# Performance work log

Measured on AMD Instinct MI355X. Metric: run time of the kernel, lower is better.

## Reference

```python
import jax, jax.numpy as jnp
import numpy as np

B, T, N, H = 512, 128, 128, 256


def setup_inputs() -> dict:
    key = jax.random.key(0)
    ks = jax.random.split(key, 8)
    rn = lambda k, shape, sc: (jax.random.normal(k, shape, jnp.float32) * sc)
    return {
        "data": rn(ks[0], (B, T, N), 1.0),
        "h0": jnp.zeros((B, H), jnp.float32),
        # SimpleRNNCell params: h_t = tanh(x@Wx + h@Wh + b)
        "Wx": rn(ks[1], (N, H), 0.05),
        "Wh": rn(ks[2], (H, H), 0.05),
        "b": jnp.zeros((H,), jnp.float32),
        # InputAttention: w1: Dense(T) over last dim T; w2: Dense(T) over hidden; v: Dense(1)
        "W1": rn(ks[3], (T, T), 0.05),
        "b1": jnp.zeros((T,), jnp.float32),
        "W2": rn(ks[4], (H, T), 0.05),
        "b2": jnp.zeros((T,), jnp.float32),
        "Wv": rn(ks[5], (T, 1), 0.05),
        "bv": jnp.zeros((1,), jnp.float32),
        "n": N,
    }


def reference(data, h0, Wx, Wh, b, W1, b1, W2, b2, Wv, bv, n):
    # data: (B, T, n); h0: (B, H)
    Tlen = data.shape[1]
    x_perm = jnp.swapaxes(data, 1, 2)          # (B, n, T) == Permute((2,1))(x)
    pre = x_perm @ W1 + b1                      # w1(x_perm): loop-invariant, hoisted

    def step(h, x_t):
        # SimpleRNNCell: new state used for this step's attention
        h_new = jnp.tanh(x_t @ Wx + h @ Wh + b)                 # (B, H)
        q = h_new @ W2 + b2                                      # w2(RepeatVector(n)(h)) per row -> (B, T)
        score = jnp.tanh(pre + q[:, None, :])                    # (B, n, T)
        e = score @ Wv + bv                                      # (B, n, 1)
        e = jnp.swapaxes(e, 1, 2)                                # Permute((2,1)) -> (B, 1, n)
        alpha = jax.nn.softmax(e, axis=-1)                       # softmax over n
        return h_new, alpha

    xs = jnp.swapaxes(data, 0, 1)               # (T, B, n): data[:, t, :] per step
    _, alphas = jax.lax.scan(step, h0, xs)      # (T, B, 1, n)
    # faithful to tf.reshape(alpha_seq.stack(), (-1, T, n))
    alpha_seq = alphas.reshape(-1, Tlen, n)     # (B, T, n)
    return data * alpha_seq
```

## Files before the change

### kernel.cpp

```cpp
#include <hip/hip_runtime.h>


#define C2L 2.8853900817779268f
#define L2E 1.4426950408889634f

typedef _Float16 hf;
typedef _Float16 hf2 __attribute__((ext_vector_type(2)));
typedef _Float16 hf4 __attribute__((ext_vector_type(4)));
typedef _Float16 hf8 __attribute__((ext_vector_type(8)));
typedef float f32x4 __attribute__((ext_vector_type(4)));

__device__ __forceinline__ float fast_exp2(float x){
#if __has_builtin(__builtin_amdgcn_exp2f)
  return __builtin_amdgcn_exp2f(x);
#else
  return exp2f(x);
#endif
}
__device__ __forceinline__ float fast_rcp(float x){
#if __has_builtin(__builtin_amdgcn_rcpf)
  return __builtin_amdgcn_rcpf(x);
#else
  return 1.f/x;
#endif
}
__device__ __forceinline__ float dot2f(hf2 a, hf2 b, float c){
#if __has_builtin(__builtin_amdgcn_fdot2)
  return __builtin_amdgcn_fdot2(a, b, c, false);
#else
  return c + (float)a.x*(float)b.x + (float)a.y*(float)b.y;
#endif
}

__global__ __launch_bounds__(256) void k_prep_w(const float* __restrict__ Wx,
    const float* __restrict__ W2, const float* __restrict__ W1,
    hf* __restrict__ wts){
  int tid = blockIdx.x*256 + threadIdx.x;
  if (tid < 32768){
    int n = tid >> 7, k = tid & 127;
    wts[tid] = (hf)Wx[k*256 + n];
  } else if (tid < 65536){
    int t2 = tid - 32768;
    int n = t2 >> 8, k = t2 & 255;
    wts[tid] = (hf)W2[k*128 + n];
  } else {
    int t3 = tid - 65536;
    int n = t3 >> 7, k = t3 & 127;
    wts[tid] = (hf)W1[k*128 + n];
  }
}

template<int K, int MODE>
__global__ __launch_bounds__(256) void k_gemm(const void* __restrict__ Asrc,
    const hf* __restrict__ Bt, const float* __restrict__ bias,
    float* __restrict__ Cout){
  constexpr int SA = 136;
  __shared__ alignas(16) hf As[64*SA];
  __shared__ alignas(16) hf Bs[128*SA];
  const int tid = threadIdx.x;
  const int w = tid >> 6, lane = tid & 63;
  const int c = lane & 15, q = lane >> 4;
  const int bx = blockIdx.x;
  const int col0 = (MODE==0) ? blockIdx.y*128 : 0;

  float br[8];
  #pragma unroll
  for (int ni=0; ni<8; ni++) br[ni] = bias[col0 + ni*16 + c];

  f32x4 acc[8];
  #pragma unroll
  for (int ni=0; ni<8; ni++) acc[ni] = (f32x4){0.f,0.f,0.f,0.f};

  for (int kc=0; kc<K/128; kc++){
    if (MODE == 0){
      const float* A = (const float*)Asrc + (long)bx*64*128;
      #pragma unroll
      for (int v=0; v<8; v++){
        int f4 = v*256 + tid;
        int m = f4 >> 5, k4 = (f4 & 31)*4;
        float4 d = *(const float4*)&A[m*128 + k4];
        hf4 h = {(hf)d.x,(hf)d.y,(hf)d.z,(hf)d.w};
        *(hf4*)&As[m*SA + k4] = h;
      }
    } else if (MODE == 1){
      const hf* A = (const hf*)Asrc + (long)bx*64*256;
      #pragma unroll
      for (int v=0; v<4; v++){
        int f8 = v*256 + tid;
        int m = f8 >> 4, k8 = (f8 & 15)*8;
        *(hf8*)&As[m*SA + k8] = *(const hf8*)&A[m*256 + kc*128 + k8];
      }
    } else {
      const float* A = (const float*)Asrc + (long)(bx>>1)*16384;
      const int i0 = (bx & 1)*64;
      #pragma unroll
      for (int v=0; v<8; v++){
        int f4 = v*256 + tid;
        int t = f4 >> 4, i4 = (f4 & 15)*4;
        float4 d = *(const float4*)&A[t*128 + i0 + i4];
        As[(i4+0)*SA + t] = (hf)d.x;
        As[(i4+1)*SA + t] = (hf)d.y;
        As[(i4+2)*SA + t] = (hf)d.z;
        As[(i4+3)*SA + t] = (hf)d.w;
      }
    }
    #pragma unroll
    for (int v=0; v<8; v++){
      int f8 = v*256 + tid;
      int n = f8 >> 4, k8 = (f8 & 15)*8;
      *(hf8*)&Bs[n*SA + k8] = *(const hf8*)&Bt[(col0+n)*K + kc*128 + k8];
    }
    __syncthreads();
    #pragma unroll
    for (int kk=0; kk<4; kk++){
      hf8 a = *(const hf8*)&As[(w*16 + c)*SA + kk*32 + q*8];
      #pragma unroll
      for (int ni=0; ni<8; ni++){
        hf8 b = *(const hf8*)&Bs[(ni*16 + c)*SA + kk*32 + q*8];
        acc[ni] = __builtin_amdgcn_mfma_f32_16x16x32_f16(a, b, acc[ni], 0, 0, 0);
      }
    }
    __syncthreads();
  }
  #pragma unroll
  for (int ni=0; ni<8; ni++){
    #pragma unroll
    for (int r=0; r<4; r++){
      int rloc = w*16 + q*4 + r;
      int col = col0 + ni*16 + c;
      float val = acc[ni][r] + br[ni];
      int addr;
      if (MODE == 0){
        int R = bx*64 + rloc;
        int b_ = R >> 7, t_ = R & 127;
        addr = (t_*512 + b_)*256 + col;
      } else if (MODE == 1){
        int R = bx*64 + rloc;
        addr = R*128 + col;
        val = fast_exp2(C2L*val);
      } else {
        int b_ = bx >> 1, i_ = (bx & 1)*64 + rloc;
        addr = b_*16384 + i_*128 + col;
        val = fast_exp2(C2L*val);
      }
      Cout[addr] = val;
    }
  }
}

__global__ __launch_bounds__(512) void k_rnn(const float* __restrict__ h0,
    const float* __restrict__ Wh, const float* __restrict__ xw,
    hf* __restrict__ Hb){
  __shared__ alignas(16) hf h_s[2][2][256];
  const int tid = threadIdx.x;
  const int j = tid & 255, beta = tid >> 8;
  const int bb = blockIdx.x*2 + beta;
  hf2 wreg[128];
  #pragma unroll
  for (int m=0;m<128;m++){
    float w0 = Wh[(2*m)*256 + j];
    float w1 = Wh[(2*m+1)*256 + j];
    wreg[m] = (hf2){(hf)w0, (hf)w1};
  }
  h_s[0][beta][j] = (hf)h0[bb*256 + j];
  float z = xw[(0*512 + bb)*256 + j];
  __syncthreads();
  for (int t=0;t<128;t++){
    int p = t & 1;
    float zn = (t < 127) ? xw[((t+1)*512 + bb)*256 + j] : 0.f;
    const hf2* hp = (const hf2*)(&h_s[p][beta][0]);
    float a0=0.f,a1=0.f,a2=0.f,a3=0.f;
    #pragma unroll
    for (int m=0;m<128;m+=4){
      a0 = dot2f(wreg[m],   hp[m],   a0);
      a1 = dot2f(wreg[m+1], hp[m+1], a1);
      a2 = dot2f(wreg[m+2], hp[m+2], a2);
      a3 = dot2f(wreg[m+3], hp[m+3], a3);
    }
    float v = z + ((a0+a1)+(a2+a3));
    float e2 = fast_exp2(v*C2L);
    float hn = 1.f - 2.f*fast_rcp(e2 + 1.f);
    Hb[(t*512+bb)*256 + j] = (hf)hn;
    h_s[p^1][beta][j] = (hf)hn;
    z = zn;
    __syncthreads();
  }
}

__global__ __launch_bounds__(256, 4) void k_attn(const float* __restrict__ P,
    const float* __restrict__ Qm, const float* __restrict__ Wv,
    const float* __restrict__ data, float* __restrict__ out){
  __shared__ alignas(16) float qs[32*128];
  __shared__ alignas(16) float wvs[128];
  __shared__ alignas(16) float epart[2][2][2][128];
  __shared__ float red[2][2][2];
  const int b = blockIdx.x, tile = blockIdx.y;
  const int tid = threadIdx.x;
  const int i = tid & 127, hl = tid >> 7;
  const int t0 = tile*32;
  if (tid < 128) wvs[tid] = -2.f*Wv[tid];
  #pragma unroll
  for (int v=0; v<4; v++){
    int flat = v*1024 + tid*4;
    int tt = flat >> 7, c = flat & 127;
    *(float4*)&qs[flat] = *(const float4*)&Qm[((t0+tt)*512 + b)*128 + c];
  }
  float4 p4[16];
  const float* prow = P + b*16384 + i*128 + hl*64;
  #pragma unroll
  for (int v=0; v<16; v++) p4[v] = *(const float4*)&prow[v*4];
  __syncthreads();
  for (int tp=0; tp<16; tp++){
    const int pp = tp & 1;
    const float* q0r = &qs[(2*tp)*128   + hl*64];
    const float* q1r = &qs[(2*tp+1)*128 + hl*64];
    const float* wvr = &wvs[hl*64];
    float4 acc0 = {0.f,0.f,0.f,0.f}, acc1 = {0.f,0.f,0.f,0.f};
    #pragma unroll
    for (int m=0; m<16; m++){
      float4 Pv = p4[m];
      float4 q0 = *(const float4*)&q0r[m*4];
      float4 q1 = *(const float4*)&q1r[m*4];
      float4 wv = *(const float4*)&wvr[m*4];
      float r0x = fast_rcp(fmaf(Pv.x, q0.x, 1.f));
      float r0y = fast_rcp(fmaf(Pv.y, q0.y, 1.f));
      float r0z = fast_rcp(fmaf(Pv.z, q0.z, 1.f));
      float r0w = fast_rcp(fmaf(Pv.w, q0.w, 1.f));
      float r1x = fast_rcp(fmaf(Pv.x, q1.x, 1.f));
      float r1y = fast_rcp(fmaf(Pv.y, q1.y, 1.f));
      float r1z = fast_rcp(fmaf(Pv.z, q1.z, 1.f));
      float r1w = fast_rcp(fmaf(Pv.w, q1.w, 1.f));
      acc0.x = fmaf(wv.x, r0x, acc0.x);
      acc0.y = fmaf(wv.y, r0y, acc0.y);
      acc0.z = fmaf(wv.z, r0z, acc0.z);
      acc0.w = fmaf(wv.w, r0w, acc0.w);
      acc1.x = fmaf(wv.x, r1x, acc1.x);
      acc1.y = fmaf(wv.y, r1y, acc1.y);
      acc1.z = fmaf(wv.z, r1z, acc1.z);
      acc1.w = fmaf(wv.w, r1w, acc1.w);
    }
    epart[pp][0][hl][i] = (acc0.x+acc0.y)+(acc0.z+acc0.w);
    epart[pp][1][hl][i] = (acc1.x+acc1.y)+(acc1.z+acc1.w);
    __syncthreads();
    const int tpar = tid >> 7;
    float e = epart[pp][tpar][0][i] + epart[pp][tpar][1][i];
    float pexp = fast_exp2(e*L2E);
    float sm = pexp;
    #pragma unroll
    for (int off=32; off; off>>=1) sm += __shfl_xor(sm, off);
    if ((tid & 63) == 0) red[pp][tpar][(tid>>6)&1] = sm;
    __syncthreads();
    float ssum = red[pp][tpar][0] + red[pp][tpar][1];
    float alpha = pexp * fast_rcp(ssum);
    int t = t0 + 2*tp + tpar;
    int base = (t*512 + b)*128 + i;
    out[base] = data[base]*alpha;
  }
}

extern "C" void kernel_launch(void* const* d_in, const int* in_sizes, int n_in,
                              void* d_out, int out_size, void* d_ws, size_t ws_size,
                              hipStream_t stream) {
  const float* data = (const float*)d_in[0];
  const float* h0   = (const float*)d_in[1];
  const float* Wx   = (const float*)d_in[2];
  const float* Wh   = (const float*)d_in[3];
  const float* bb   = (const float*)d_in[4];
  const float* W1   = (const float*)d_in[5];
  const float* b1   = (const float*)d_in[6];
  const float* W2   = (const float*)d_in[7];
  const float* b2   = (const float*)d_in[8];
  const float* Wv   = (const float*)d_in[9];
  float* wsp = (float*)d_ws;
  float* P   = wsp;
  float* xwQ = wsp + 8388608;
  hf*    Hbf = (hf*)(wsp + 25165824);
  hf*    wts = (hf*)(wsp + 33554432);
  const hf* Wxt = wts;
  const hf* W2t = wts + 32768;
  const hf* W1t = wts + 65536;
  float* out = (float*)d_out;

  hipLaunchKernelGGL(k_prep_w, dim3(320), dim3(256), 0, stream, Wx, W2, W1, wts);
  hipLaunchKernelGGL((k_gemm<128,0>), dim3(1024,2), dim3(256), 0, stream,
                     (const void*)data, Wxt, bb, xwQ);
  hipLaunchKernelGGL((k_gemm<128,2>), dim3(1024),   dim3(256), 0, stream,
                     (const void*)data, W1t, b1, P);
  hipLaunchKernelGGL(k_rnn, dim3(256), dim3(512), 0, stream, h0, Wh, xwQ, Hbf);
  hipLaunchKernelGGL((k_gemm<256,1>), dim3(1024),   dim3(256), 0, stream,
                     (const void*)Hbf, W2t, b2, xwQ);
  hipLaunchKernelGGL(k_attn, dim3(512, 4), dim3(256), 0, stream, P, xwQ, Wv, data, out);
}
```

Baseline: 399.2 us.

## Split RNN to one batch per block and pair reciprocals in attention

Result: faster. 385.5 us (-3.4%).

```diff
diff --git a/kernel.cpp b/kernel.cpp
--- a/kernel.cpp
+++ b/kernel.cpp
@@ -148,13 +148,12 @@
   }
 }
 
-__global__ __launch_bounds__(512) void k_rnn(const float* __restrict__ h0,
+__global__ __launch_bounds__(256, 3) void k_rnn(const float* __restrict__ h0,
     const float* __restrict__ Wh, const float* __restrict__ xw,
     hf* __restrict__ Hb){
-  __shared__ alignas(16) hf h_s[2][2][256];
-  const int tid = threadIdx.x;
-  const int j = tid & 255, beta = tid >> 8;
-  const int bb = blockIdx.x*2 + beta;
+  __shared__ alignas(16) hf h_s[2][256];
+  const int j = threadIdx.x;
+  const int bb = blockIdx.x;
   hf2 wreg[128];
   #pragma unroll
   for (int m=0;m<128;m++){
@@ -162,26 +161,31 @@
     float w1 = Wh[(2*m+1)*256 + j];
     wreg[m] = (hf2){(hf)w0, (hf)w1};
   }
-  h_s[0][beta][j] = (hf)h0[bb*256 + j];
+  h_s[0][j] = (hf)h0[bb*256 + j];
   float z = xw[(0*512 + bb)*256 + j];
   __syncthreads();
   for (int t=0;t<128;t++){
     int p = t & 1;
     float zn = (t < 127) ? xw[((t+1)*512 + bb)*256 + j] : 0.f;
-    const hf2* hp = (const hf2*)(&h_s[p][beta][0]);
-    float a0=0.f,a1=0.f,a2=0.f,a3=0.f;
-    #pragma unroll
-    for (int m=0;m<128;m+=4){
-      a0 = dot2f(wreg[m],   hp[m],   a0);
-      a1 = dot2f(wreg[m+1], hp[m+1], a1);
-      a2 = dot2f(wreg[m+2], hp[m+2], a2);
-      a3 = dot2f(wreg[m+3], hp[m+3], a3);
-    }
-    float v = z + ((a0+a1)+(a2+a3));
+    const hf8* h8 = (const hf8*)(&h_s[p][0]);
+    float a[8];
+    #pragma unroll
+    for (int u=0;u<8;u++) a[u]=0.f;
+    #pragma unroll
+    for (int mm=0; mm<32; mm++){
+      hf8 hv = h8[mm];
+      hf2 h0p = {hv[0],hv[1]}, h1p = {hv[2],hv[3]};
+      hf2 h2p = {hv[4],hv[5]}, h3p = {hv[6],hv[7]};
+      a[(4*mm+0)&7] = dot2f(wreg[4*mm+0], h0p, a[(4*mm+0)&7]);
+      a[(4*mm+1)&7] = dot2f(wreg[4*mm+1], h1p, a[(4*mm+1)&7]);
+      a[(4*mm+2)&7] = dot2f(wreg[4*mm+2], h2p, a[(4*mm+2)&7]);
+      a[(4*mm+3)&7] = dot2f(wreg[4*mm+3], h3p, a[(4*mm+3)&7]);
+    }
+    float v = z + (((a[0]+a[1])+(a[2]+a[3])) + ((a[4]+a[5])+(a[6]+a[7])));
     float e2 = fast_exp2(v*C2L);
     float hn = 1.f - 2.f*fast_rcp(e2 + 1.f);
     Hb[(t*512+bb)*256 + j] = (hf)hn;
-    h_s[p^1][beta][j] = (hf)hn;
+    h_s[p^1][j] = (hf)hn;
     z = zn;
     __syncthreads();
   }
@@ -192,8 +196,8 @@
     const float* __restrict__ data, float* __restrict__ out){
   __shared__ alignas(16) float qs[32*128];
   __shared__ alignas(16) float wvs[128];
-  __shared__ alignas(16) float epart[2][2][2][128];
-  __shared__ float red[2][2][2];
+  __shared__ alignas(16) float epart[2][2][4][128];
+  __shared__ float red[2][4][2];
   const int b = blockIdx.x, tile = blockIdx.y;
   const int tid = threadIdx.x;
   const int i = tid & 127, hl = tid >> 7;
@@ -210,51 +214,82 @@
   #pragma unroll
   for (int v=0; v<16; v++) p4[v] = *(const float4*)&prow[v*4];
   __syncthreads();
-  for (int tp=0; tp<16; tp++){
+  for (int tp=0; tp<8; tp++){
     const int pp = tp & 1;
-    const float* q0r = &qs[(2*tp)*128   + hl*64];
-    const float* q1r = &qs[(2*tp+1)*128 + hl*64];
+    const float* q0r = &qs[(4*tp)*128   + hl*64];
+    const float* q1r = &qs[(4*tp+1)*128 + hl*64];
+    const float* q2r = &qs[(4*tp+2)*128 + hl*64];
+    const float* q3r = &qs[(4*tp+3)*128 + hl*64];
     const float* wvr = &wvs[hl*64];
-    float4 acc0 = {0.f,0.f,0.f,0.f}, acc1 = {0.f,0.f,0.f,0.f};
+    float acc0=0.f, acc1=0.f, acc2=0.f, acc3=0.f;
     #pragma unroll
     for (int m=0; m<16; m++){
       float4 Pv = p4[m];
-      float4 q0 = *(const float4*)&q0r[m*4];
-      float4 q1 = *(const float4*)&q1r[m*4];
       float4 wv = *(const float4*)&wvr[m*4];
-      float r0x = fast_rcp(fmaf(Pv.x, q0.x, 1.f));
-      float r0y = fast_rcp(fmaf(Pv.y, q0.y, 1.f));
-      float r0z = fast_rcp(fmaf(Pv.z, q0.z, 1.f));
-      float r0w = fast_rcp(fmaf(Pv.w, q0.w, 1.f));
-      float r1x = fast_rcp(fmaf(Pv.x, q1.x, 1.f));
-      float r1y = fast_rcp(fmaf(Pv.y, q1.y, 1.f));
-      float r1z = fast_rcp(fmaf(Pv.z, q1.z, 1.f));
-      float r1w = fast_rcp(fmaf(Pv.w, q1.w, 1.f));
-      acc0.x = fmaf(wv.x, r0x, acc0.x);
-      acc0.y = fmaf(wv.y, r0y, acc0.y);
-      acc0.z = fmaf(wv.z, r0z, acc0.z);
-      acc0.w = fmaf(wv.w, r0w, acc0.w);
-      acc1.x = fmaf(wv.x, r1x, acc1.x);
-      acc1.y = fmaf(wv.y, r1y, acc1.y);
-      acc1.z = fmaf(wv.z, r1z, acc1.z);
-      acc1.w = fmaf(wv.w, r1w, acc1.w);
-    }
-    epart[pp][0][hl][i] = (acc0.x+acc0.y)+(acc0.z+acc0.w);
-    epart[pp][1][hl][i] = (acc1.x+acc1.y)+(acc1.z+acc1.w);
-    __syncthreads();
-    const int tpar = tid >> 7;
-    float e = epart[pp][tpar][0][i] + epart[pp][tpar][1][i];
-    float pexp = fast_exp2(e*L2E);
-    float sm = pexp;
-    #pragma unroll
-    for (int off=32; off; off>>=1) sm += __shfl_xor(sm, off);
-    if ((tid & 63) == 0) red[pp][tpar][(tid>>6)&1] = sm;
-    __syncthreads();
-    float ssum = red[pp][tpar][0] + red[pp][tpar][1];
-    float alpha = pexp * fast_rcp(ssum);
-    int t = t0 + 2*tp + tpar;
-    int base = (t*512 + b)*128 + i;
-    out[base] = data[base]*alpha;
+      {
+        float4 qq = *(const float4*)&q0r[m*4];
+        float u = fmaf(Pv.x, qq.x, 1.f), v = fmaf(Pv.y, qq.y, 1.f);
+        float n = fmaf(wv.x, v, wv.y*u);
+        acc0 = fmaf(n, fast_rcp(u*v), acc0);
+        float u2 = fmaf(Pv.z, qq.z, 1.f), v2 = fmaf(Pv.w, qq.w, 1.f);
+        float n2 = fmaf(wv.z, v2, wv.w*u2);
+        acc0 = fmaf(n2, fast_rcp(u2*v2), acc0);
+      }
+      {
+        float4 qq = *(const float4*)&q1r[m*4];
+        float u = fmaf(Pv.x, qq.x, 1.f), v = fmaf(Pv.y, qq.y, 1.f);
+        float n = fmaf(wv.x, v, wv.y*u);
+        acc1 = fmaf(n, fast_rcp(u*v), acc1);
+        float u2 = fmaf(Pv.z, qq.z, 1.f), v2 = fmaf(Pv.w, qq.w, 1.f);
+        float n2 = fmaf(wv.z, v2, wv.w*u2);
+        acc1 = fmaf(n2, fast_rcp(u2*v2), acc1);
+      }
+      {
+        float4 qq = *(const float4*)&q2r[m*4];
+        float u = fmaf(Pv.x, qq.x, 1.f), v = fmaf(Pv.y, qq.y, 1.f);
+        float n = fmaf(wv.x, v, wv.y*u);
+        acc2 = fmaf(n, fast_rcp(u*v), acc2);
+        float u2 = fmaf(Pv.z, qq.z, 1.f), v2 = fmaf(Pv.w, qq.w, 1.f);
+        float n2 = fmaf(wv.z, v2, wv.w*u2);
+        acc2 = fmaf(n2, fast_rcp(u2*v2), acc2);
+      }
+      {
+        float4 qq = *(const float4*)&q3r[m*4];
+        float u = fmaf(Pv.x, qq.x, 1.f), v = fmaf(Pv.y, qq.y, 1.f);
+        float n = fmaf(wv.x, v, wv.y*u);
+        acc3 = fmaf(n, fast_rcp(u*v), acc3);
+        float u2 = fmaf(Pv.z, qq.z, 1.f), v2 = fmaf(Pv.w, qq.w, 1.f);
+        float n2 = fmaf(wv.z, v2, wv.w*u2);
+        acc3 = fmaf(n2, fast_rcp(u2*v2), acc3);
+      }
+    }
+    epart[pp][hl][0][i] = acc0;
+    epart[pp][hl][1][i] = acc1;
+    epart[pp][hl][2][i] = acc2;
+    epart[pp][hl][3][i] = acc3;
+    __syncthreads();
+    const int g = tid >> 7;
+    float pe[2];
+    #pragma unroll
+    for (int s=0; s<2; s++){
+      int tl = g + 2*s;
+      float e = epart[pp][0][tl][i] + epart[pp][1][tl][i];
+      pe[s] = fast_exp2(e*L2E);
+      float sm = pe[s];
+      #pragma unroll
+      for (int off=32; off; off>>=1) sm += __shfl_xor(sm, off);
+      if ((tid & 63) == 0) red[pp][tl][(tid>>6)&1] = sm;
+    }
+    __syncthreads();
+    #pragma unroll
+    for (int s=0; s<2; s++){
+      int tl = g + 2*s;
+      float ssum = red[pp][tl][0] + red[pp][tl][1];
+      float alpha = pe[s] * fast_rcp(ssum);
+      int t = t0 + 4*tp + tl;
+      int base = (t*512 + b)*128 + i;
+      out[base] = data[base]*alpha;
+    }
   }
 }
 
@@ -286,7 +321,7 @@
                      (const void*)data, Wxt, bb, xwQ);
   hipLaunchKernelGGL((k_gemm<128,2>), dim3(1024),   dim3(256), 0, stream,
                      (const void*)data, W1t, b1, P);
-  hipLaunchKernelGGL(k_rnn, dim3(256), dim3(512), 0, stream, h0, Wh, xwQ, Hbf);
+  hipLaunchKernelGGL(k_rnn, dim3(512), dim3(256), 0, stream, h0, Wh, xwQ, Hbf);
   hipLaunchKernelGGL((k_gemm<256,1>), dim3(1024),   dim3(256), 0, stream,
                      (const void*)Hbf, W2t, b2, xwQ);
   hipLaunchKernelGGL(k_attn, dim3(512, 4), dim3(256), 0, stream, P, xwQ, Wv, data, out);
```
